# Kernel optimization log

Measured on AMD Instinct MI355X. Metric: run time of the kernel, lower is better.

Reference implementation:

```python
import jax, jax.numpy as jnp
import numpy as np

MIN_NORM = 1e-15
EPS = 4e-3  # fp32 boundary epsilon used by HGCN PoincareBall


def _norm(x):
    return jnp.maximum(jnp.linalg.norm(x, axis=-1, keepdims=True), MIN_NORM)


def _artanh(x):
    return jnp.arctanh(jnp.clip(x, -1.0 + 1e-7, 1.0 - 1e-7))


def proj(x, c):
    # clip points to the open Poincare ball of curvature c
    norm = _norm(x)
    maxnorm = (1.0 - EPS) / jnp.sqrt(c)
    return jnp.where(norm > maxnorm, x / norm * maxnorm, x)


def expmap0(u, c):
    sc = jnp.sqrt(c)
    un = _norm(u)
    return jnp.tanh(sc * un) * u / (sc * un)


def logmap0(p, c):
    sc = jnp.sqrt(c)
    pn = _norm(p)
    return _artanh(sc * pn) * p / (pn * sc)


def mobius_add(x, y, c):
    x2 = jnp.sum(x * x, axis=-1, keepdims=True)
    y2 = jnp.sum(y * y, axis=-1, keepdims=True)
    xy = jnp.sum(x * y, axis=-1, keepdims=True)
    num = (1.0 + 2.0 * c * xy + c * y2) * x + (1.0 - c * x2) * y
    den = 1.0 + 2.0 * c * xy + (c ** 2) * x2 * y2
    return num / jnp.maximum(den, MIN_NORM)


def _mobius_from_mx(mx, x, c):
    # shared tail of mobius_matvec: mx is the Euclidean product, x the input points
    sc = jnp.sqrt(c)
    x_norm = _norm(x)            # [..., 1]
    mx_norm = _norm(mx)          # [..., 1]
    res = jnp.tanh(mx_norm / x_norm * _artanh(sc * x_norm)) * mx / (mx_norm * sc)
    zero_row = jnp.all(mx == 0, axis=-1, keepdims=True)
    return jnp.where(zero_row, jnp.zeros_like(res), res)


def mobius_matvec(m, x, c):
    # standard form: mx = x @ m^T   (m: [out, in], x: [N, in])
    return _mobius_from_mx(x @ m.T, x, c)


def hyp_linear(x, W, b, c):
    hw = proj(expmap0(W, c), c)             # proj_tan0 is identity on PoincareBall
    res = proj(mobius_matvec(hw, x, c), c)
    hb = proj(expmap0(b[None, :], c), c)
    return proj(mobius_add(res, hb, c), c)


def hyp_agg(h, adj, W, b, c):
    hw = proj(expmap0(W, c), c)
    support = mobius_matvec(hw, h, c)       # [N, O]
    # mobius_matvec(support, adj, c): Euclidean part is adj @ support,
    # hyperbolic rescale uses row norms of adj (the 'x' argument)
    out = _mobius_from_mx(adj @ support, adj, c)
    out = mobius_add(out, b[None, :], c)    # raw Euclidean bias, as in source
    return proj(out, c)


def hyp_act(h, c):
    xt = jax.nn.leaky_relu(logmap0(h, c))   # default slope 0.01 == F.leaky_relu
    return proj(expmap0(xt, c), 1.0 - c)    # NOTE: source projects with 1-c


def setup_inputs() -> dict:
    key = jax.random.key(0)
    kx, ka, kw1, kw2, kb2 = jax.random.split(key, 5)
    N, IN, OUT = 8192, 512, 128
    x = jax.random.normal(kx, (N, IN), dtype=jnp.float32) * 0.1
    adj = jax.random.uniform(ka, (N, N), dtype=jnp.float32) * (1.0 / N)
    c = jnp.full((1,), 0.7, dtype=jnp.float32)
    glorot = np.sqrt(6.0 / (IN + OUT))
    lin_weight = jax.random.uniform(kw1, (OUT, IN), minval=-glorot, maxval=glorot, dtype=jnp.float32)
    lin_bias = jnp.zeros((OUT,), dtype=jnp.float32)
    stdv = 1.0 / np.sqrt(OUT)
    agg_weight = jax.random.uniform(kw2, (OUT, OUT), minval=-stdv, maxval=stdv, dtype=jnp.float32)
    agg_bias = jax.random.uniform(kb2, (OUT,), minval=-stdv, maxval=stdv, dtype=jnp.float32)
    return {"x": x, "adj": adj, "c": c, "lin_weight": lin_weight, "lin_bias": lin_bias,
            "agg_weight": agg_weight, "agg_bias": agg_bias}


def reference(x, adj, c, lin_weight, lin_bias, agg_weight, agg_bias):
    h = hyp_linear(x, lin_weight, lin_bias, c)
    h = hyp_agg(h, adj, agg_weight, agg_bias, c)
    return hyp_act(h, c)
```

## Files before the change

kernel.cpp:

```cpp
#include <hip/hip_runtime.h>
#include <math.h>


#define MINN 1e-15f

typedef __bf16 bf16x8 __attribute__((ext_vector_type(8)));
typedef float  f32x4  __attribute__((ext_vector_type(4)));

__device__ __forceinline__ unsigned short f2bf(float f) {
  unsigned int u = __float_as_uint(f);
  u += 0x7FFFu + ((u >> 16) & 1u);
  return (unsigned short)(u >> 16);
}

__device__ __forceinline__ float artanh_clip(float z) {
  const float B = (float)(1.0 - 1e-7);
  z = fminf(fmaxf(z, -B), B);
  return 0.5f * logf((1.0f + z) / (1.0f - z));
}

__device__ __forceinline__ float red16(float v) {
  v += __shfl_xor(v, 1, 16);
  v += __shfl_xor(v, 2, 16);
  v += __shfl_xor(v, 4, 16);
  v += __shfl_xor(v, 8, 16);
  return v;
}
__device__ __forceinline__ int red16_and(int v) {
  v &= __shfl_xor(v, 1, 16);
  v &= __shfl_xor(v, 2, 16);
  v &= __shfl_xor(v, 4, 16);
  v &= __shfl_xor(v, 8, 16);
  return v;
}

__device__ __forceinline__ float block_reduce_128(float v, float* red, int t) {
  #pragma unroll
  for (int m = 1; m < 64; m <<= 1) v += __shfl_xor(v, m, 64);
  if ((t & 63) == 0) red[t >> 6] = v;
  __syncthreads();
  return red[0] + red[1];
}

__device__ __forceinline__ size_t bswz(int k, int n) {
  return ((size_t)(((k >> 5) * 8 + (n >> 4)) * 64 + ((k >> 3) & 3) * 16 +
                   (n & 15))) * 8 + (k & 7);
}

__global__ __launch_bounds__(128) void prep_kernel(
    const float* __restrict__ lw, const float* __restrict__ aw,
    const float* __restrict__ lb, const float* __restrict__ cp,
    unsigned short* __restrict__ B1, unsigned short* __restrict__ B2,
    float* __restrict__ hb)
{
  const float c  = cp[0];
  const float sc = sqrtf(c);
  const float maxn = 0.996f / sc;
  const int b = blockIdx.x, t = threadIdx.x;
  __shared__ float red[2];

  if (b < 128) {
    const int o = b;
    float4 v = ((const float4*)(lw + (size_t)o * 512))[t];
    float ss = block_reduce_128(v.x*v.x + v.y*v.y + v.z*v.z + v.w*v.w, red, t);
    float un = fmaxf(sqrtf(ss), MINN);
    float f  = tanhf(sc * un) / (sc * un);
    float nn = f * un;
    if (nn > maxn) f *= maxn / nn;
    float vals[4] = {v.x, v.y, v.z, v.w};
    #pragma unroll
    for (int i = 0; i < 4; ++i)
      B1[bswz(4 * t + i, o)] = f2bf(f * vals[i]);
  } else if (b < 256) {
    const int n = b - 128;
    float v = aw[(size_t)n * 128 + t];
    float ss = block_reduce_128(v * v, red, t);
    float un = fmaxf(sqrtf(ss), MINN);
    float f  = tanhf(sc * un) / (sc * un);
    float nn = f * un;
    if (nn > maxn) f *= maxn / nn;
    B2[bswz(t, n)] = f2bf(f * v);
  } else {
    float v = lb[t];
    float ss = block_reduce_128(v * v, red, t);
    float un = fmaxf(sqrtf(ss), MINN);
    float f  = tanhf(sc * un) / (sc * un);
    float nn = f * un;
    if (nn > maxn) f *= maxn / nn;
    hb[t] = f * v;
  }
}

template <int MODE>
__global__ __launch_bounds__(256, 2) void hyp_gemm(
    const float* __restrict__ A, const bf16x8* __restrict__ Bf, int K,
    const float* __restrict__ cp, const float* __restrict__ yvec,
    void* __restrict__ outp)
{
  __shared__ float part[4][16][132];
  __shared__ float asw[4][16];
  const int t    = threadIdx.x;
  const int w    = t >> 6, lane = t & 63;
  const int quad = lane >> 4, l15 = lane & 15;
  const int row0 = blockIdx.x * 16;
  const float c  = cp[0];
  const float sc = sqrtf(c);
  const float maxn = 0.996f / sc;

  const int Kw     = K >> 2;
  const int nsteps = Kw >> 5;
  const int k0w    = w * Kw;

  f32x4 acc[8] = {};
  float asum = 0.f;

  const float*  Ap = A + (size_t)(row0 + l15) * K + k0w + quad * 8;
  const bf16x8* Bp = Bf + (size_t)(k0w >> 5) * 512 + lane;

  float4 a0 = *(const float4*)(Ap);
  float4 a1 = *(const float4*)(Ap + 4);
  bf16x8 b[8];
  #pragma unroll
  for (int i = 0; i < 8; ++i) b[i] = Bp[i * 64];

  for (int s = 0; s < nsteps; ++s) {
    float4 na0, na1; bf16x8 nb[8];
    const bool more = (s + 1 < nsteps);
    if (more) {
      const float* Ap2 = Ap + (size_t)(s + 1) * 32;
      na0 = *(const float4*)(Ap2);
      na1 = *(const float4*)(Ap2 + 4);
      const bf16x8* Bp2 = Bp + (size_t)(s + 1) * 512;
      #pragma unroll
      for (int i = 0; i < 8; ++i) nb[i] = Bp2[i * 64];
    }
    asum += a0.x*a0.x + a0.y*a0.y + a0.z*a0.z + a0.w*a0.w
          + a1.x*a1.x + a1.y*a1.y + a1.z*a1.z + a1.w*a1.w;
    union { unsigned short u[8]; bf16x8 v; } pk;
    pk.u[0] = f2bf(a0.x); pk.u[1] = f2bf(a0.y);
    pk.u[2] = f2bf(a0.z); pk.u[3] = f2bf(a0.w);
    pk.u[4] = f2bf(a1.x); pk.u[5] = f2bf(a1.y);
    pk.u[6] = f2bf(a1.z); pk.u[7] = f2bf(a1.w);
    #pragma unroll
    for (int i = 0; i < 8; ++i)
      acc[i] = __builtin_amdgcn_mfma_f32_16x16x32_bf16(pk.v, b[i], acc[i],
                                                       0, 0, 0);
    if (more) {
      a0 = na0; a1 = na1;
      #pragma unroll
      for (int i = 0; i < 8; ++i) b[i] = nb[i];
    }
  }

  asum += __shfl_xor(asum, 16, 64);
  asum += __shfl_xor(asum, 32, 64);
  #pragma unroll
  for (int i = 0; i < 8; ++i)
    #pragma unroll
    for (int r = 0; r < 4; ++r)
      part[w][quad * 4 + r][i * 16 + l15] = acc[i][r];
  if (lane < 16) asw[w][l15] = asum;
  __syncthreads();

  const int row = t >> 4, j0 = t & 15;
  float v[8];
  #pragma unroll
  for (int i = 0; i < 8; ++i)
    v[i] = part[0][row][j0 * 8 + i] + part[1][row][j0 * 8 + i]
         + part[2][row][j0 * 8 + i] + part[3][row][j0 * 8 + i];
  const float xss = asw[0][row] + asw[1][row] + asw[2][row] + asw[3][row];

  float mxss_l = 0.f; int zf = 1;
  #pragma unroll
  for (int i = 0; i < 8; ++i) { mxss_l += v[i] * v[i]; zf &= (v[i] == 0.f); }
  const float mxss = red16(mxss_l);
  zf = red16_and(zf);

  const float xn  = fmaxf(sqrtf(xss), MINN);
  const float mxn = fmaxf(sqrtf(mxss), MINN);
  float f1 = 0.f;
  if (!zf) f1 = tanhf(mxn / xn * artanh_clip(sc * xn)) / (mxn * sc);

  if (MODE == 2) {
    const int k = row0 + row;
    unsigned short* Bo = (unsigned short*)outp;
    const size_t base = ((size_t)(((k >> 5) * 8 + (j0 >> 1)) * 64 +
                         ((k >> 3) & 3) * 16 + 8 * (j0 & 1))) * 8 + (k & 7);
    #pragma unroll
    for (int i = 0; i < 8; ++i)
      Bo[base + (size_t)i * 8] = f2bf(f1 * v[i]);
    return;
  }

  float yv[8];
  {
    float4 q0 = ((const float4*)yvec)[j0 * 2];
    float4 q1 = ((const float4*)yvec)[j0 * 2 + 1];
    yv[0]=q0.x; yv[1]=q0.y; yv[2]=q0.z; yv[3]=q0.w;
    yv[4]=q1.x; yv[5]=q1.y; yv[6]=q1.z; yv[7]=q1.w;
  }

  float g = f1;
  if (MODE == 1) {
    float rn = f1 * mxn;
    if (rn > maxn) g = f1 * (maxn / rn);
  }

  float xy_l = 0.f, y2_l = 0.f;
  float o8[8];
  #pragma unroll
  for (int i = 0; i < 8; ++i) {
    o8[i] = g * v[i];
    xy_l += o8[i] * yv[i];
    y2_l += yv[i] * yv[i];
  }
  const float xy = red16(xy_l), y2 = red16(y2_l);
  const float x2 = g * g * mxss;
  const float den = fmaxf(1.0f + 2.0f * c * xy + c * c * x2 * y2, MINN);
  const float ca = (1.0f + 2.0f * c * xy + c * y2) / den;
  const float cb = (1.0f - c * x2) / den;
  float h8[8]; float hss_l = 0.f;
  #pragma unroll
  for (int i = 0; i < 8; ++i) {
    h8[i] = ca * o8[i] + cb * yv[i];
    hss_l += h8[i] * h8[i];
  }
  const float hss = red16(hss_l);
  const float hn  = fmaxf(sqrtf(hss), MINN);
  const float s2  = (hn > maxn) ? maxn / hn : 1.0f;

  float* orow = (float*)outp + (size_t)(row0 + row) * 128 + j0 * 8;

  if (MODE == 1) {
    float4 o0 = make_float4(s2*h8[0], s2*h8[1], s2*h8[2], s2*h8[3]);
    float4 o1 = make_float4(s2*h8[4], s2*h8[5], s2*h8[6], s2*h8[7]);
    *(float4*)orow = o0; *(float4*)(orow + 4) = o1;
    return;
  }

  const float pn = fmaxf(s2 * hn, MINN);
  const float lf = artanh_clip(sc * pn) / (pn * sc);
  float xt[8]; float uss_l = 0.f;
  #pragma unroll
  for (int i = 0; i < 8; ++i) {
    float l = lf * (s2 * h8[i]);
    xt[i] = (l >= 0.f) ? l : 0.01f * l;
    uss_l += xt[i] * xt[i];
  }
  const float uss = red16(uss_l);
  const float un  = fmaxf(sqrtf(uss), MINN);
  const float ef  = tanhf(sc * un) / (sc * un);
  const float on  = ef * un;
  const float maxn2 = 0.996f / sqrtf(1.0f - c);
  const float s3 = (on > maxn2) ? maxn2 / on : 1.0f;
  float4 o0 = make_float4(s3*ef*xt[0], s3*ef*xt[1], s3*ef*xt[2], s3*ef*xt[3]);
  float4 o1 = make_float4(s3*ef*xt[4], s3*ef*xt[5], s3*ef*xt[6], s3*ef*xt[7]);
  *(float4*)orow = o0; *(float4*)(orow + 4) = o1;
}

extern "C" void kernel_launch(void* const* d_in, const int* in_sizes, int n_in,
                              void* d_out, int out_size, void* d_ws, size_t ws_size,
                              hipStream_t stream)
{
  const float* x   = (const float*)d_in[0];
  const float* adj = (const float*)d_in[1];
  const float* cp  = (const float*)d_in[2];
  const float* lw  = (const float*)d_in[3];
  const float* lb  = (const float*)d_in[4];
  const float* aw  = (const float*)d_in[5];
  const float* ab  = (const float*)d_in[6];
  float* out = (float*)d_out;

  char* ws = (char*)d_ws;
  unsigned short* B1sw = (unsigned short*)(ws);
  unsigned short* B2sw = (unsigned short*)(ws + 131072);
  unsigned short* B3sw = (unsigned short*)(ws + 163840);
  float*          hb   = (float*)(ws + 2260992);
  float*          h    = (float*)(ws + 2261504);

  prep_kernel<<<257, 128, 0, stream>>>(lw, aw, lb, cp, B1sw, B2sw, hb);
  hyp_gemm<1><<<512, 256, 0, stream>>>(x,   (const bf16x8*)B1sw, 512,  cp, hb, h);
  hyp_gemm<2><<<512, 256, 0, stream>>>(h,   (const bf16x8*)B2sw, 128,  cp, nullptr, B3sw);
  hyp_gemm<3><<<512, 256, 0, stream>>>(adj, (const bf16x8*)B3sw, 8192, cp, ab, out);
}
```

Baseline: 438.0 us.

## Fuse first two hyperbolic GEMMs and deepen pipelining in adjacency GEMM

Merges the linear layer and the support GEMM into one kernel, which keeps the intermediate h in LDS as bf16 and no longer writes it to global memory. The large adj GEMM is rewritten to cover 32 rows per block with a 2-way K split, an 8-deep A prefetch and 4-deep B prefetch, and truncating bf16 packing through a perm instruction in place of round-to-nearest. This targets memory latency on the 256MB adj read and removes one launch. The cost is higher register pressure (launch bounds drop to 1 block per CU), and truncation adds slightly more precision error.

```diff
diff --git a/kernel.cpp b/kernel.cpp
--- a/kernel.cpp
+++ b/kernel.cpp
@@ -11,6 +11,11 @@
   unsigned int u = __float_as_uint(f);
   u += 0x7FFFu + ((u >> 16) & 1u);
   return (unsigned short)(u >> 16);
+}
+
+__device__ __forceinline__ unsigned pk_trunc(float lo, float hi) {
+  return __builtin_amdgcn_perm(__float_as_uint(hi), __float_as_uint(lo),
+                               0x07060302u);
 }
 
 __device__ __forceinline__ float artanh_clip(float z) {
@@ -31,6 +36,18 @@
   v &= __shfl_xor(v, 2, 16);
   v &= __shfl_xor(v, 4, 16);
   v &= __shfl_xor(v, 8, 16);
+  return v;
+}
+__device__ __forceinline__ float red8(float v) {
+  v += __shfl_xor(v, 1, 8);
+  v += __shfl_xor(v, 2, 8);
+  v += __shfl_xor(v, 4, 8);
+  return v;
+}
+__device__ __forceinline__ int red8_and(int v) {
+  v &= __shfl_xor(v, 1, 8);
+  v &= __shfl_xor(v, 2, 8);
+  v &= __shfl_xor(v, 4, 8);
   return v;
 }
 
@@ -91,67 +108,44 @@
   }
 }
 
-template <int MODE>
-__global__ __launch_bounds__(256, 2) void hyp_gemm(
-    const float* __restrict__ A, const bf16x8* __restrict__ Bf, int K,
-    const float* __restrict__ cp, const float* __restrict__ yvec,
-    void* __restrict__ outp)
+__global__ __launch_bounds__(256, 2) void hyp_fused12(
+    const float* __restrict__ x, const bf16x8* __restrict__ B1f,
+    const bf16x8* __restrict__ B2f, const float* __restrict__ cp,
+    const float* __restrict__ hbv, unsigned short* __restrict__ B3)
 {
-  __shared__ float part[4][16][132];
+  __shared__ __align__(16) float part[4][16][132];
   __shared__ float asw[4][16];
-  const int t    = threadIdx.x;
-  const int w    = t >> 6, lane = t & 63;
+  __shared__ __align__(16) unsigned short h_lds[16][136];
+  const int t = threadIdx.x;
+  const int w = t >> 6, lane = t & 63;
   const int quad = lane >> 4, l15 = lane & 15;
   const int row0 = blockIdx.x * 16;
-  const float c  = cp[0];
-  const float sc = sqrtf(c);
-  const float maxn = 0.996f / sc;
-
-  const int Kw     = K >> 2;
-  const int nsteps = Kw >> 5;
-  const int k0w    = w * Kw;
+  const float c = cp[0], sc = sqrtf(c), maxn = 0.996f / sc;
 
   f32x4 acc[8] = {};
-  float asum = 0.f;
-
-  const float*  Ap = A + (size_t)(row0 + l15) * K + k0w + quad * 8;
-  const bf16x8* Bp = Bf + (size_t)(k0w >> 5) * 512 + lane;
-
-  float4 a0 = *(const float4*)(Ap);
-  float4 a1 = *(const float4*)(Ap + 4);
-  bf16x8 b[8];
-  #pragma unroll
-  for (int i = 0; i < 8; ++i) b[i] = Bp[i * 64];
-
-  for (int s = 0; s < nsteps; ++s) {
-    float4 na0, na1; bf16x8 nb[8];
-    const bool more = (s + 1 < nsteps);
-    if (more) {
-      const float* Ap2 = Ap + (size_t)(s + 1) * 32;
-      na0 = *(const float4*)(Ap2);
-      na1 = *(const float4*)(Ap2 + 4);
-      const bf16x8* Bp2 = Bp + (size_t)(s + 1) * 512;
-      #pragma unroll
-      for (int i = 0; i < 8; ++i) nb[i] = Bp2[i * 64];
-    }
-    asum += a0.x*a0.x + a0.y*a0.y + a0.z*a0.z + a0.w*a0.w
-          + a1.x*a1.x + a1.y*a1.y + a1.z*a1.z + a1.w*a1.w;
-    union { unsigned short u[8]; bf16x8 v; } pk;
-    pk.u[0] = f2bf(a0.x); pk.u[1] = f2bf(a0.y);
-    pk.u[2] = f2bf(a0.z); pk.u[3] = f2bf(a0.w);
-    pk.u[4] = f2bf(a1.x); pk.u[5] = f2bf(a1.y);
-    pk.u[6] = f2bf(a1.z); pk.u[7] = f2bf(a1.w);
+  float as4[4] = {};
+  const float*  Ap = x + (size_t)(row0 + l15) * 512 + w * 128 + quad * 8;
+  const bf16x8* Bp = B1f + (size_t)(w * 4) * 512 + lane;
+
+  #pragma unroll
+  for (int s = 0; s < 4; ++s) {
+    float4 x0 = *(const float4*)(Ap + s * 32);
+    float4 x1 = *(const float4*)(Ap + s * 32 + 4);
+    as4[0] = fmaf(x0.x, x0.x, fmaf(x0.y, x0.y, as4[0]));
+    as4[1] = fmaf(x0.z, x0.z, fmaf(x0.w, x0.w, as4[1]));
+    as4[2] = fmaf(x1.x, x1.x, fmaf(x1.y, x1.y, as4[2]));
+    as4[3] = fmaf(x1.z, x1.z, fmaf(x1.w, x1.w, as4[3]));
+    union { unsigned short us[8]; bf16x8 v; } pk;
+    pk.us[0] = f2bf(x0.x); pk.us[1] = f2bf(x0.y);
+    pk.us[2] = f2bf(x0.z); pk.us[3] = f2bf(x0.w);
+    pk.us[4] = f2bf(x1.x); pk.us[5] = f2bf(x1.y);
+    pk.us[6] = f2bf(x1.z); pk.us[7] = f2bf(x1.w);
     #pragma unroll
     for (int i = 0; i < 8; ++i)
-      acc[i] = __builtin_amdgcn_mfma_f32_16x16x32_bf16(pk.v, b[i], acc[i],
-                                                       0, 0, 0);
-    if (more) {
-      a0 = na0; a1 = na1;
-      #pragma unroll
-      for (int i = 0; i < 8; ++i) b[i] = nb[i];
-    }
-  }
-
+      acc[i] = __builtin_amdgcn_mfma_f32_16x16x32_bf16(
+                   pk.v, Bp[(size_t)s * 512 + i * 64], acc[i], 0, 0, 0);
+  }
+  float asum = (as4[0] + as4[1]) + (as4[2] + as4[3]);
   asum += __shfl_xor(asum, 16, 64);
   asum += __shfl_xor(asum, 32, 64);
   #pragma unroll
@@ -181,33 +175,19 @@
   float f1 = 0.f;
   if (!zf) f1 = tanhf(mxn / xn * artanh_clip(sc * xn)) / (mxn * sc);
 
-  if (MODE == 2) {
-    const int k = row0 + row;
-    unsigned short* Bo = (unsigned short*)outp;
-    const size_t base = ((size_t)(((k >> 5) * 8 + (j0 >> 1)) * 64 +
-                         ((k >> 3) & 3) * 16 + 8 * (j0 & 1))) * 8 + (k & 7);
-    #pragma unroll
-    for (int i = 0; i < 8; ++i)
-      Bo[base + (size_t)i * 8] = f2bf(f1 * v[i]);
-    return;
-  }
-
+  float g = f1;
+  {
+    float rn = f1 * mxn;
+    if (rn > maxn) g = f1 * (maxn / rn);
+  }
   float yv[8];
   {
-    float4 q0 = ((const float4*)yvec)[j0 * 2];
-    float4 q1 = ((const float4*)yvec)[j0 * 2 + 1];
+    float4 q0 = ((const float4*)hbv)[j0 * 2];
+    float4 q1 = ((const float4*)hbv)[j0 * 2 + 1];
     yv[0]=q0.x; yv[1]=q0.y; yv[2]=q0.z; yv[3]=q0.w;
     yv[4]=q1.x; yv[5]=q1.y; yv[6]=q1.z; yv[7]=q1.w;
   }
-
-  float g = f1;
-  if (MODE == 1) {
-    float rn = f1 * mxn;
-    if (rn > maxn) g = f1 * (maxn / rn);
-  }
-
-  float xy_l = 0.f, y2_l = 0.f;
-  float o8[8];
+  float xy_l = 0.f, y2_l = 0.f, o8[8];
   #pragma unroll
   for (int i = 0; i < 8; ++i) {
     o8[i] = g * v[i];
@@ -228,34 +208,209 @@
   const float hss = red16(hss_l);
   const float hn  = fmaxf(sqrtf(hss), MINN);
   const float s2  = (hn > maxn) ? maxn / hn : 1.0f;
-
-  float* orow = (float*)outp + (size_t)(row0 + row) * 128 + j0 * 8;
-
-  if (MODE == 1) {
-    float4 o0 = make_float4(s2*h8[0], s2*h8[1], s2*h8[2], s2*h8[3]);
-    float4 o1 = make_float4(s2*h8[4], s2*h8[5], s2*h8[6], s2*h8[7]);
-    *(float4*)orow = o0; *(float4*)(orow + 4) = o1;
-    return;
-  }
+  const float hn2 = fmaxf(s2 * hn, MINN);
+
+  {
+    union { unsigned short us[8]; uint4 q; } hp;
+    #pragma unroll
+    for (int i = 0; i < 8; ++i) hp.us[i] = f2bf(s2 * h8[i]);
+    *(uint4*)&h_lds[row][j0 * 8] = hp.q;
+  }
+  __syncthreads();
+
+  const bf16x8 av2 = *(const bf16x8*)&h_lds[l15][w * 32 + quad * 8];
+  f32x4 acc2[8] = {};
+  #pragma unroll
+  for (int i = 0; i < 8; ++i)
+    acc2[i] = __builtin_amdgcn_mfma_f32_16x16x32_bf16(
+                  av2, B2f[(size_t)(w * 8 + i) * 64 + lane], acc2[i], 0, 0, 0);
+  #pragma unroll
+  for (int i = 0; i < 8; ++i)
+    #pragma unroll
+    for (int r = 0; r < 4; ++r)
+      part[w][quad * 4 + r][i * 16 + l15] = acc2[i][r];
+  __syncthreads();
+
+  float v2[8];
+  #pragma unroll
+  for (int i = 0; i < 8; ++i)
+    v2[i] = part[0][row][j0 * 8 + i] + part[1][row][j0 * 8 + i]
+          + part[2][row][j0 * 8 + i] + part[3][row][j0 * 8 + i];
+  float m2l = 0.f; int zf2 = 1;
+  #pragma unroll
+  for (int i = 0; i < 8; ++i) { m2l += v2[i] * v2[i]; zf2 &= (v2[i] == 0.f); }
+  const float mx2ss = red16(m2l);
+  zf2 = red16_and(zf2);
+  const float mx2n = fmaxf(sqrtf(mx2ss), MINN);
+  float f2 = 0.f;
+  if (!zf2) f2 = tanhf(mx2n / hn2 * artanh_clip(sc * hn2)) / (mx2n * sc);
+
+  const int k = row0 + row;
+  const size_t base = ((size_t)(((k >> 5) * 8 + (j0 >> 1)) * 64 +
+                       ((k >> 3) & 3) * 16 + 8 * (j0 & 1))) * 8 + (k & 7);
+  #pragma unroll
+  for (int i = 0; i < 8; ++i)
+    B3[base + (size_t)i * 8] = f2bf(f2 * v2[i]);
+}
+
+#define G3_COMPUTE(U)                                                        \
+  {                                                                          \
+    float4 x0 = a0[U], x1 = a1[U];                                           \
+    as4[0] = fmaf(x0.x, x0.x, fmaf(x0.y, x0.y, as4[0]));                     \
+    as4[1] = fmaf(x0.z, x0.z, fmaf(x0.w, x0.w, as4[1]));                     \
+    as4[2] = fmaf(x1.x, x1.x, fmaf(x1.y, x1.y, as4[2]));                     \
+    as4[3] = fmaf(x1.z, x1.z, fmaf(x1.w, x1.w, as4[3]));                     \
+    union { unsigned u32[4]; bf16x8 v; } pk;                                 \
+    pk.u32[0] = pk_trunc(x0.x, x0.y);                                        \
+    pk.u32[1] = pk_trunc(x0.z, x0.w);                                        \
+    pk.u32[2] = pk_trunc(x1.x, x1.y);                                        \
+    pk.u32[3] = pk_trunc(x1.z, x1.w);                                        \
+    _Pragma("unroll")                                                        \
+    for (int i = 0; i < 8; ++i)                                              \
+      acc[i] = __builtin_amdgcn_mfma_f32_16x16x32_bf16(pk.v, b[(U) & 3][i],  \
+                                                       acc[i], 0, 0, 0);     \
+  }
+
+__global__ __launch_bounds__(256, 1) void hyp_gemm3(
+    const float* __restrict__ A, const bf16x8* __restrict__ Bf,
+    const float* __restrict__ cp, const float* __restrict__ yvec,
+    float* __restrict__ out)
+{
+  __shared__ __align__(16) float part[4][16][132];
+  __shared__ float asw[4][16];
+  const int t = threadIdx.x;
+  const int w = t >> 6, lane = t & 63;
+  const int quad = lane >> 4, l15 = lane & 15;
+  const int rh = w >> 1, kh = w & 1;
+  const int rowbase = blockIdx.x * 32;
+  const int row0 = rowbase + rh * 16;
+  const float c = cp[0], sc = sqrtf(c), maxn = 0.996f / sc;
+
+  const int k0w = kh * 4096;
+  f32x4 acc[8] = {};
+  float as4[4] = {};
+  const float*  Ap = A + (size_t)(row0 + l15) * 8192 + k0w + quad * 8;
+  const bf16x8* Bp = Bf + (size_t)(k0w >> 5) * 512 + lane;
+
+  float4 a0[8], a1[8];
+  bf16x8 b[4][8];
+  #pragma unroll
+  for (int p = 0; p < 8; ++p) {
+    a0[p] = *(const float4*)(Ap + p * 32);
+    a1[p] = *(const float4*)(Ap + p * 32 + 4);
+  }
+  #pragma unroll
+  for (int p = 0; p < 4; ++p)
+    #pragma unroll
+    for (int i = 0; i < 8; ++i) b[p][i] = Bp[(size_t)p * 512 + i * 64];
+
+  for (int s = 0; s < 120; s += 8) {
+    #pragma unroll
+    for (int u = 0; u < 8; ++u) {
+      const int sv = s + u;
+      G3_COMPUTE(u);
+      a0[u] = *(const float4*)(Ap + (size_t)(sv + 8) * 32);
+      a1[u] = *(const float4*)(Ap + (size_t)(sv + 8) * 32 + 4);
+      #pragma unroll
+      for (int i = 0; i < 8; ++i)
+        b[u & 3][i] = Bp[(size_t)(sv + 4) * 512 + i * 64];
+    }
+  }
+  #pragma unroll
+  for (int u = 0; u < 8; ++u) {
+    G3_COMPUTE(u);
+    if (u < 4) {
+      #pragma unroll
+      for (int i = 0; i < 8; ++i)
+        b[u & 3][i] = Bp[(size_t)(124 + u) * 512 + i * 64];
+    }
+  }
+
+  float asum = (as4[0] + as4[1]) + (as4[2] + as4[3]);
+  asum += __shfl_xor(asum, 16, 64);
+  asum += __shfl_xor(asum, 32, 64);
+  #pragma unroll
+  for (int i = 0; i < 8; ++i)
+    #pragma unroll
+    for (int r = 0; r < 4; ++r)
+      part[w][quad * 4 + r][i * 16 + l15] = acc[i][r];
+  if (lane < 16) asw[w][l15] = asum;
+  __syncthreads();
+
+  const int row = t >> 3, j0 = t & 7;
+  const int rh2 = row >> 4, rr = row & 15;
+  float v[16];
+  #pragma unroll
+  for (int i = 0; i < 4; ++i) {
+    float4 qa = *(const float4*)&part[rh2 * 2][rr][j0 * 16 + 4 * i];
+    float4 qb = *(const float4*)&part[rh2 * 2 + 1][rr][j0 * 16 + 4 * i];
+    v[4*i+0] = qa.x + qb.x; v[4*i+1] = qa.y + qb.y;
+    v[4*i+2] = qa.z + qb.z; v[4*i+3] = qa.w + qb.w;
+  }
+  const float xss = asw[rh2 * 2][rr] + asw[rh2 * 2 + 1][rr];
+
+  float mxss_l = 0.f; int zf = 1;
+  #pragma unroll
+  for (int i = 0; i < 16; ++i) { mxss_l += v[i] * v[i]; zf &= (v[i] == 0.f); }
+  const float mxss = red8(mxss_l);
+  zf = red8_and(zf);
+
+  const float xn  = fmaxf(sqrtf(xss), MINN);
+  const float mxn = fmaxf(sqrtf(mxss), MINN);
+  float f1 = 0.f;
+  if (!zf) f1 = tanhf(mxn / xn * artanh_clip(sc * xn)) / (mxn * sc);
+
+  float yv[16];
+  #pragma unroll
+  for (int i = 0; i < 4; ++i) {
+    float4 q = ((const float4*)yvec)[j0 * 4 + i];
+    yv[4*i+0] = q.x; yv[4*i+1] = q.y; yv[4*i+2] = q.z; yv[4*i+3] = q.w;
+  }
+
+  float xy_l = 0.f, y2_l = 0.f, o16[16];
+  #pragma unroll
+  for (int i = 0; i < 16; ++i) {
+    o16[i] = f1 * v[i];
+    xy_l += o16[i] * yv[i];
+    y2_l += yv[i] * yv[i];
+  }
+  const float xy = red8(xy_l), y2 = red8(y2_l);
+  const float x2 = f1 * f1 * mxss;
+  const float den = fmaxf(1.0f + 2.0f * c * xy + c * c * x2 * y2, MINN);
+  const float ca = (1.0f + 2.0f * c * xy + c * y2) / den;
+  const float cb = (1.0f - c * x2) / den;
+  float h16[16]; float hss_l = 0.f;
+  #pragma unroll
+  for (int i = 0; i < 16; ++i) {
+    h16[i] = ca * o16[i] + cb * yv[i];
+    hss_l += h16[i] * h16[i];
+  }
+  const float hss = red8(hss_l);
+  const float hn  = fmaxf(sqrtf(hss), MINN);
+  const float s2  = (hn > maxn) ? maxn / hn : 1.0f;
 
   const float pn = fmaxf(s2 * hn, MINN);
   const float lf = artanh_clip(sc * pn) / (pn * sc);
-  float xt[8]; float uss_l = 0.f;
-  #pragma unroll
-  for (int i = 0; i < 8; ++i) {
-    float l = lf * (s2 * h8[i]);
+  float xt[16]; float uss_l = 0.f;
+  #pragma unroll
+  for (int i = 0; i < 16; ++i) {
+    float l = lf * (s2 * h16[i]);
     xt[i] = (l >= 0.f) ? l : 0.01f * l;
     uss_l += xt[i] * xt[i];
   }
-  const float uss = red16(uss_l);
+  const float uss = red8(uss_l);
   const float un  = fmaxf(sqrtf(uss), MINN);
   const float ef  = tanhf(sc * un) / (sc * un);
   const float on  = ef * un;
   const float maxn2 = 0.996f / sqrtf(1.0f - c);
   const float s3 = (on > maxn2) ? maxn2 / on : 1.0f;
-  float4 o0 = make_float4(s3*ef*xt[0], s3*ef*xt[1], s3*ef*xt[2], s3*ef*xt[3]);
-  float4 o1 = make_float4(s3*ef*xt[4], s3*ef*xt[5], s3*ef*xt[6], s3*ef*xt[7]);
-  *(float4*)orow = o0; *(float4*)(orow + 4) = o1;
+
+  float* orow = out + (size_t)(rowbase + row) * 128 + j0 * 16;
+  #pragma unroll
+  for (int i = 0; i < 4; ++i)
+    *(float4*)(orow + 4 * i) = make_float4(
+        s3 * ef * xt[4*i+0], s3 * ef * xt[4*i+1],
+        s3 * ef * xt[4*i+2], s3 * ef * xt[4*i+3]);
 }
 
 extern "C" void kernel_launch(void* const* d_in, const int* in_sizes, int n_in,
@@ -276,10 +431,9 @@
   unsigned short* B2sw = (unsigned short*)(ws + 131072);
   unsigned short* B3sw = (unsigned short*)(ws + 163840);
   float*          hb   = (float*)(ws + 2260992);
-  float*          h    = (float*)(ws + 2261504);
 
   prep_kernel<<<257, 128, 0, stream>>>(lw, aw, lb, cp, B1sw, B2sw, hb);
-  hyp_gemm<1><<<512, 256, 0, stream>>>(x,   (const bf16x8*)B1sw, 512,  cp, hb, h);
-  hyp_gemm<2><<<512, 256, 0, stream>>>(h,   (const bf16x8*)B2sw, 128,  cp, nullptr, B3sw);
-  hyp_gemm<3><<<512, 256, 0, stream>>>(adj, (const bf16x8*)B3sw, 8192, cp, ab, out);
-}
+  hyp_fused12<<<512, 256, 0, stream>>>(x, (const bf16x8*)B1sw,
+                                       (const bf16x8*)B2sw, cp, hb, B3sw);
+  hyp_gemm3<<<256, 256, 0, stream>>>(adj, (const bf16x8*)B3sw, cp, ab, out);
+}
```

Result: no change. 436.2 us (-0.4%).
